# Optimization experiments

Hardware: AMD Instinct MI355X
Metric: run time of the kernel (lower is better)

The kernel has to match this reference:

```python
import jax, jax.numpy as jnp
import numpy as np

N, E, IN, H, D, C = 30000, 400000, 128, 4, 64, 40
EPS = 1e-5
SLOPE = 0.2  # DGL GATv2Conv leaky_relu negative_slope default


def setup_inputs() -> dict:
    key = jax.random.key(0)
    ks = jax.random.split(key, 20)
    def rn(k, shape, s=0.05):
        return jax.random.normal(k, shape, jnp.float32) * s
    return {
        "x": jax.random.normal(ks[0], (N, IN), jnp.float32),
        "src": jax.random.randint(ks[1], (E,), 0, N),
        "dst": jax.random.randint(ks[2], (E,), 0, N),
        # layer 0: in=128 -> heads*64 (residual projection since 128 != 256)
        "W_src0": rn(ks[3], (IN, H * D)), "W_dst0": rn(ks[4], (IN, H * D)),
        "b0": jnp.zeros((H * D,), jnp.float32), "attn0": rn(ks[5], (H, D)),
        "res_W0": rn(ks[6], (IN, H * D)),
        # layer 1: 256 -> heads*64 (identity residual since 256 == 256)
        "W_src1": rn(ks[7], (H * D, H * D)), "W_dst1": rn(ks[8], (H * D, H * D)),
        "b1": jnp.zeros((H * D,), jnp.float32), "attn1": rn(ks[9], (H, D)),
        # layer 2: 256 -> heads*40 (residual projection)
        "W_src2": rn(ks[10], (H * D, H * C)), "W_dst2": rn(ks[11], (H * D, H * C)),
        "b2": jnp.zeros((H * C,), jnp.float32), "attn2": rn(ks[12], (H, C)),
        "res_W2": rn(ks[13], (H * D, H * C)),
        # batchnorm affine params (training-mode batch stats)
        "g0": jnp.ones((H * D,), jnp.float32), "be0": jnp.zeros((H * D,), jnp.float32),
        "g1": jnp.ones((H * D,), jnp.float32), "be1": jnp.zeros((H * D,), jnp.float32),
    }


def gatv2_layer(h, src, dst, Wsrc, Wdst, b, attn, resW, out_dim, relu_act):
    # DGL GATv2Conv: score_e = attn . leaky_relu(fc_src(h)[u] + fc_dst(h)[v])
    n = h.shape[0]
    fs = (h @ Wsrc).reshape(n, H, out_dim)
    fd = (h @ Wdst).reshape(n, H, out_dim)
    e = jax.nn.leaky_relu(fs[src] + fd[dst], SLOPE)      # [E, H, out]
    score = jnp.einsum("ehd,hd->eh", e, attn)            # [E, H]
    # segment softmax over incoming edges of each dst node
    m = jax.ops.segment_max(score, dst, num_segments=n)
    m = jnp.where(jnp.isfinite(m), m, 0.0)               # zero in-degree safety
    ex = jnp.exp(score - m[dst])
    denom = jax.ops.segment_sum(ex, dst, num_segments=n)
    alpha = ex / jnp.maximum(denom, 1e-9)[dst]
    rst = jax.ops.segment_sum(alpha[:, :, None] * fs[src], dst, num_segments=n)
    res = (h @ resW).reshape(n, H, out_dim) if resW is not None else h.reshape(n, H, out_dim)
    rst = rst + res + b.reshape(1, H, out_dim)
    return jax.nn.relu(rst) if relu_act else rst


def batchnorm(h, g, be):
    mu = h.mean(0)
    var = h.var(0)  # biased variance, as torch BN uses for normalization
    return g * (h - mu) * jax.lax.rsqrt(var + EPS) + be


def reference(x, src, dst, W_src0, W_dst0, b0, attn0, res_W0, W_src1, W_dst1, b1, attn1, W_src2, W_dst2, b2, attn2, res_W2, g0, be0, g1, be1):
    h = gatv2_layer(x, src, dst, W_src0, W_dst0, b0, attn0, res_W0, D, True)
    h = jax.nn.relu(batchnorm(h.reshape(N, H * D), g0, be0))  # dropout = identity (eval)
    h = gatv2_layer(h, src, dst, W_src1, W_dst1, b1, attn1, None, D, True)
    h = jax.nn.relu(batchnorm(h.reshape(N, H * D), g1, be1))
    h = gatv2_layer(h, src, dst, W_src2, W_dst2, b2, attn2, res_W2, C, False)
    h = h.mean(1)  # mean over heads -> [N, C]
    return jax.nn.log_softmax(h, axis=-1)
```

## Files before the change

### kernel.cpp

```cpp
#include <hip/hip_runtime.h>
#include <hip/hip_bf16.h>
#include <math.h>

#define NN 30000
#define EE 400000
#define INP 128
#define HH 4
#define DD 64
#define CC 40
#define HD 256
#define HC 160
#define NBLK 118

typedef unsigned short ushort;
typedef __attribute__((ext_vector_type(8))) short s8v;
typedef __attribute__((ext_vector_type(4))) float f4v;


__device__ inline ushort bf16_of_float(float f) {
    __hip_bfloat16 b = __float2bfloat16(f);
    return *(ushort*)&b;
}
__device__ __forceinline__ float2 cvt2(unsigned d) {
    return make_float2(__uint_as_float(d << 16), __uint_as_float(d & 0xFFFF0000u));
}
__device__ __forceinline__ float b2f(ushort u) { return __uint_as_float(((unsigned)u) << 16); }

__device__ __forceinline__ float2 f2add(float2 a, float2 b){ return make_float2(a.x+b.x, a.y+b.y); }
__device__ __forceinline__ float2 f2mul(float2 a, float2 b){ return make_float2(a.x*b.x, a.y*b.y); }
__device__ __forceinline__ float2 f2muls(float2 a, float s){ return make_float2(a.x*s, a.y*s); }
__device__ __forceinline__ float2 f2max(float2 a, float2 b){ return make_float2(fmaxf(a.x,b.x), fmaxf(a.y,b.y)); }
__device__ __forceinline__ float2 f2fma(float2 a, float2 b, float2 c){
    return make_float2(__fmaf_rn(a.x,b.x,c.x), __fmaf_rn(a.y,b.y,c.y));
}

__device__ __forceinline__ void gld16(const void* g, void* l) {
    __builtin_amdgcn_global_load_lds((const __attribute__((address_space(1))) void*)g,
                                     (__attribute__((address_space(3))) void*)l, 16, 0, 0);
}

__device__ __forceinline__ float rowsum16(float x) {
    int t;
    t = __builtin_amdgcn_update_dpp(0, __float_as_int(x), 0x128, 0xF, 0xF, false); x += __int_as_float(t);
    t = __builtin_amdgcn_update_dpp(0, __float_as_int(x), 0x124, 0xF, 0xF, false); x += __int_as_float(t);
    t = __builtin_amdgcn_update_dpp(0, __float_as_int(x), 0x122, 0xF, 0xF, false); x += __int_as_float(t);
    t = __builtin_amdgcn_update_dpp(0, __float_as_int(x), 0x121, 0xF, 0xF, false); x += __int_as_float(t);
    return x;
}
__device__ __forceinline__ float rowmax16(float x) {
    int t;
    t = __builtin_amdgcn_update_dpp(0, __float_as_int(x), 0x128, 0xF, 0xF, false); x = fmaxf(x, __int_as_float(t));
    t = __builtin_amdgcn_update_dpp(0, __float_as_int(x), 0x124, 0xF, 0xF, false); x = fmaxf(x, __int_as_float(t));
    t = __builtin_amdgcn_update_dpp(0, __float_as_int(x), 0x122, 0xF, 0xF, false); x = fmaxf(x, __int_as_float(t));
    t = __builtin_amdgcn_update_dpp(0, __float_as_int(x), 0x121, 0xF, 0xF, false); x = fmaxf(x, __int_as_float(t));
    return x;
}

#define XB 3750
#define TB 1408
#define ZB 240

__global__ __launch_bounds__(256) void k_prep(const float* __restrict__ x, ushort* __restrict__ xc,
        const float* W0, const float* W1, const float* W2, const float* W3,
        const float* W4, const float* W5, const float* W6, const float* W7,
        ushort* bt0, ushort* bt1, ushort* bt2,
        int* __restrict__ zero_region,
        const float* b0, const float* a0, const float* b1, const float* a1,
        const float* b2, const float* a2, const float* g0, const float* be0,
        const float* g1, const float* be1, ushort* __restrict__ smallv) {
    int b = blockIdx.x, t = threadIdx.x;
    if (b < XB) {
        int i = b * 256 + t;
        if (i < NN * INP / 4) {
            float4 v = ((const float4*)x)[i];
            ushort4 o;
            o.x = bf16_of_float(v.x); o.y = bf16_of_float(v.y);
            o.z = bf16_of_float(v.z); o.w = bf16_of_float(v.w);
            ((ushort4*)xc)[i] = o;
        }
    } else if (b < XB + TB) {
        const float* Ws[8] = {W0, W1, W2, W3, W4, W5, W6, W7};
        int g = (b - XB) * 256 + t;
        if (g < 98304) {
            int seg = g >> 15, local = g & 32767;
            int n = local >> 7, k = local & 127;
            bt0[g] = bf16_of_float(Ws[seg][k * 256 + n]);
        } else if (g < 229376) {
            int gg = g - 98304;
            int seg = gg >> 16, local = gg & 65535;
            int n = local >> 8, k = local & 255;
            bt1[gg] = bf16_of_float(Ws[3 + seg][k * 256 + n]);
        } else if (g < 360448) {
            int gg = g - 229376;
            int n = gg >> 8, k = gg & 255;
            ushort val = 0;
            if (n < 480) {
                int seg = n / 160;
                int nn = n - seg * 160;
                val = bf16_of_float(Ws[5 + seg][k * 160 + nn]);
            }
            bt2[gg] = val;
        }
    } else if (b < XB + TB + ZB) {
        int i = (b - XB - TB) * 256 + t;
        if (i < 1024 + 2 * NN + 192) zero_region[i] = 0;
    } else {
        const float* ptrs[10] = {b0, a0, b1, a1, b2, a2, g0, be0, g1, be1};
        const int sz[10] = {256, 256, 256, 256, 160, 160, 256, 256, 256, 256};
        int off = 0;
        for (int j = 0; j < 10; j++) {
            if (t < sz[j]) smallv[off + t] = bf16_of_float(ptrs[j][t]);
            off += sz[j];
        }
    }
}


__global__ __launch_bounds__(256) void k_hist(const int* __restrict__ dst, int* __restrict__ cnt) {
    int e = blockIdx.x * 256 + threadIdx.x;
    if (e < EE) atomicAdd(&cnt[dst[e]], 1);
}

__global__ __launch_bounds__(256) void k_binbeg(const int* __restrict__ cnt, int* __restrict__ binCnt,
                                                int* __restrict__ beg, int* __restrict__ total) {
    __shared__ int lb[64];
    __shared__ int ss[256];
    __shared__ int base;
    int t = threadIdx.x;
    if (t < 64) lb[t] = 0;
    __syncthreads();
    int i = blockIdx.x * 256 + t;
    int c = (i < NN) ? cnt[i] : 0;
    if (i < NN) atomicAdd(&lb[63 - min(c, 63)], 1);
    ss[t] = c;
    __syncthreads();
    if (t < 64 && lb[t] > 0) atomicAdd(&binCnt[t], lb[t]);
    for (int o = 1; o < 256; o <<= 1) {
        int v = (t >= o) ? ss[t - o] : 0;
        __syncthreads();
        ss[t] += v;
        __syncthreads();
    }
    if (t == 255) base = atomicAdd(total, ss[255]);
    __syncthreads();
    if (i < NN) beg[i] = base + ss[t] - c;
}

__global__ __launch_bounds__(256) void k_orderscatter(const int* __restrict__ cnt, const int* __restrict__ binCnt,
                                                      int* __restrict__ binPos, int* __restrict__ order,
                                                      const int* __restrict__ src, const int* __restrict__ dst,
                                                      const int* __restrict__ beg, int* __restrict__ pos,
                                                      int* __restrict__ srcs) {
    int t = threadIdx.x;
    if (blockIdx.x < NBLK) {
        __shared__ int lb[64], lbase[64], bpre[64];
        if (t < 64) { lb[t] = 0; bpre[t] = binCnt[t]; }
        __syncthreads();
        int i = blockIdx.x * 256 + t;
        int bin = 0, rank = 0;
        if (i < NN) {
            bin = 63 - min(cnt[i], 63);
            rank = atomicAdd(&lb[bin], 1);
        }
        for (int o = 1; o < 64; o <<= 1) {
            int v = (t >= o && t < 64) ? bpre[t - o] : 0;
            __syncthreads();
            if (t < 64) bpre[t] += v;
            __syncthreads();
        }
        if (t < 64 && lb[t] > 0)
            lbase[t] = bpre[t] - binCnt[t] + atomicAdd(&binPos[t], lb[t]);
        __syncthreads();
        if (i < NN) order[lbase[bin] + rank] = i;
    } else {
        int e = (blockIdx.x - NBLK) * 256 + t;
        if (e < EE) {
            int d = dst[e];
            int p = atomicAdd(&pos[d], 1);
            srcs[beg[d] + p] = src[e];
        }
    }
}


template<int K, int SEGW, int NSEG>
__global__ __launch_bounds__(256) void k_gemm_tiled(const ushort* __restrict__ A,
                                                    const ushort* __restrict__ Bt,
                                                    ushort* __restrict__ o0, ushort* __restrict__ o1,
                                                    ushort* __restrict__ o2) {
    __shared__ ushort As[128 * 32];
    __shared__ ushort Bs[128 * 32];
    int t = threadIdx.x;
    int wave = t >> 6, lane = t & 63;
    int m = lane & 15, q = lane >> 4;
    int row0 = blockIdx.x * 128, col0 = blockIdx.y * 128;
    int wr = (wave >> 1) << 6, wc = (wave & 1) << 6;
    f4v acc[4][4] = {};
    int c1 = t, c2 = t + 256;
    int ar1 = min(row0 + (c1 >> 2), NN - 1);
    int ar2 = min(row0 + (c2 >> 2), NN - 1);
    const ushort* a1 = A + (size_t)ar1 * K + (c1 & 3) * 8;
    const ushort* a2 = A + (size_t)ar2 * K + (c2 & 3) * 8;
    const ushort* b1 = Bt + (size_t)(col0 + (c1 >> 2)) * K + (c1 & 3) * 8;
    const ushort* b2 = Bt + (size_t)(col0 + (c2 >> 2)) * K + (c2 & 3) * 8;
    int wbase = wave << 10;
    char* AsB = (char*)As;
    char* BsB = (char*)Bs;

#pragma unroll
    for (int kt = 0; kt < K; kt += 32) {
        __syncthreads();
        gld16(a1 + kt, AsB + wbase);
        gld16(a2 + kt, AsB + 4096 + wbase);
        gld16(b1 + kt, BsB + wbase);
        gld16(b2 + kt, BsB + 4096 + wbase);
        __syncthreads();
        s8v af[4], bg[4];
#pragma unroll
        for (int i = 0; i < 4; i++) af[i] = *(const s8v*)&As[(wr + i * 16 + m) * 32 + q * 8];
#pragma unroll
        for (int c = 0; c < 4; c++) bg[c] = *(const s8v*)&Bs[(wc + c * 16 + m) * 32 + q * 8];
#pragma unroll
        for (int i = 0; i < 4; i++)
#pragma unroll
            for (int c = 0; c < 4; c++)
                acc[i][c] = __builtin_amdgcn_mfma_f32_16x16x32_bf16(bg[c], af[i], acc[i][c], 0, 0, 0);
    }

#pragma unroll
    for (int c = 0; c < 4; c++) {
        int gcb = col0 + wc + c * 16;
        if (gcb < SEGW * NSEG) {
            int seg = gcb / SEGW;
            int colb = gcb - seg * SEGW + q * 4;
            ushort* op = seg == 0 ? o0 : (seg == 1 ? o1 : o2);
#pragma unroll
            for (int i = 0; i < 4; i++) {
                int gr = row0 + wr + i * 16 + m;
                if (gr < NN) {
                    ushort4 s4;
                    s4.x = bf16_of_float(acc[i][c][0]);
                    s4.y = bf16_of_float(acc[i][c][1]);
                    s4.z = bf16_of_float(acc[i][c][2]);
                    s4.w = bf16_of_float(acc[i][c][3]);
                    *(ushort4*)&op[(size_t)gr * SEGW + colb] = s4;
                }
            }
        }
    }
}


template<int DH, bool FINAL>
__global__ __launch_bounds__(256) void k_aggregate(const ushort* __restrict__ fs, const ushort* __restrict__ fd,
                                                   const ushort* __restrict__ res,
                                                   const ushort* __restrict__ attn,
                                                   const ushort* __restrict__ bias,
                                                   const int* __restrict__ beg, const int* __restrict__ cnt,
                                                   const int* __restrict__ srcs,
                                                   const int* __restrict__ order,
                                                   ushort* __restrict__ outb, float* __restrict__ outf) {
    constexpr int F = HH * DH;
    constexpr int JMAX = DH >> 2;
    int tt = threadIdx.x;
    int v = __builtin_amdgcn_readfirstlane(order[blockIdx.x * 4 + (tt >> 6)]);
    int lane = tt & 63;
    int h = lane >> 4, j = lane & 15;
    bool act = j < JMAX;
    unsigned off = h * DH + 4 * j;
    unsigned vbase = (unsigned)v * F + off;
    float2 fda = {0.f,0.f}, fdb = {0.f,0.f}, ava = {0.f,0.f}, avb = {0.f,0.f};
    if (act) {
        uint2 d = *(const uint2*)&fd[vbase];
        fda = cvt2(d.x); fdb = cvt2(d.y);
        uint2 a = *(const uint2*)&attn[off];
        const float LOG2E = 1.4426950408889634f;
        ava = f2muls(cvt2(a.x), LOG2E); avb = f2muls(cvt2(a.y), LOG2E);
    }
    float l = 0.f;
    float2 acca = {0.f,0.f}, accb = {0.f,0.f};
    int b0i = beg[v], end = b0i + cnt[v];

    auto ldrow = [&](int u, float2& ra, float2& rb) {
        ra = make_float2(0.f, 0.f); rb = make_float2(0.f, 0.f);
        if (act) {
            uint2 d = *(const uint2*)&fs[(unsigned)u * F + off];
            ra = cvt2(d.x); rb = cvt2(d.y);
        }
    };
    auto dotlr = [&](const float2& ra, const float2& rb) -> float {
        float2 t0 = f2add(ra, fda);
        float2 t1 = f2add(rb, fdb);
        t0 = f2max(t0, f2muls(t0, 0.2f));
        t1 = f2max(t1, f2muls(t1, 0.2f));
        float2 p2 = f2mul(ava, t0);
        p2 = f2fma(avb, t1, p2);
        return p2.x + p2.y;
    };
    auto quadc = [&](const float2& r0a, const float2& r0b, const float2& r1a, const float2& r1b,
                     const float2& r2a, const float2& r2b, const float2& r3a, const float2& r3b) {
        float p0 = rowsum16(dotlr(r0a, r0b));
        float p1 = rowsum16(dotlr(r1a, r1b));
        float p2 = rowsum16(dotlr(r2a, r2b));
        float p3 = rowsum16(dotlr(r3a, r3b));
        float w0 = exp2f(p0), w1 = exp2f(p1), w2 = exp2f(p2), w3 = exp2f(p3);
        l += (w0 + w1) + (w2 + w3);
        acca = f2fma(make_float2(w0, w0), r0a, acca);
        accb = f2fma(make_float2(w0, w0), r0b, accb);
        acca = f2fma(make_float2(w1, w1), r1a, acca);
        accb = f2fma(make_float2(w1, w1), r1b, accb);
        acca = f2fma(make_float2(w2, w2), r2a, acca);
        accb = f2fma(make_float2(w2, w2), r2b, accb);
        acca = f2fma(make_float2(w3, w3), r3a, acca);
        accb = f2fma(make_float2(w3, w3), r3b, accb);
    };

    int i = b0i;
    if (i + 3 < end) {
        int u0 = srcs[i], u1 = srcs[i+1], u2 = srcs[i+2], u3 = srcs[i+3];
        float2 r0a, r0b, r1a, r1b, r2a, r2b, r3a, r3b;
        ldrow(u0, r0a, r0b); ldrow(u1, r1a, r1b);
        ldrow(u2, r2a, r2b); ldrow(u3, r3a, r3b);
        for (i += 4; i + 3 < end; i += 4) {
            int n0 = srcs[i], n1 = srcs[i+1], n2 = srcs[i+2], n3 = srcs[i+3];
            float2 s0a, s0b, s1a, s1b, s2a, s2b, s3a, s3b;
            ldrow(n0, s0a, s0b); ldrow(n1, s1a, s1b);
            ldrow(n2, s2a, s2b); ldrow(n3, s3a, s3b);
            quadc(r0a, r0b, r1a, r1b, r2a, r2b, r3a, r3b);
            r0a = s0a; r0b = s0b; r1a = s1a; r1b = s1b;
            r2a = s2a; r2b = s2b; r3a = s3a; r3b = s3b;
        }
        quadc(r0a, r0b, r1a, r1b, r2a, r2b, r3a, r3b);
    }
    for (; i < end; i++) {
        float2 ra, rb;
        ldrow(srcs[i], ra, rb);
        float p0 = rowsum16(dotlr(ra, rb));
        float w0 = exp2f(p0);
        l += w0;
        acca = f2fma(make_float2(w0, w0), ra, acca);
        accb = f2fma(make_float2(w0, w0), rb, accb);
    }

    float4 o4 = {0.f, 0.f, 0.f, 0.f};
    if (act) {
        float inv = 1.f / fmaxf(l, 1e-9f);
        uint2 rr = *(const uint2*)&res[vbase];
        float2 rl = cvt2(rr.x), rh = cvt2(rr.y);
        uint2 bb = *(const uint2*)&bias[off];
        float2 bl = cvt2(bb.x), bh = cvt2(bb.y);
        o4.x = acca.x * inv + rl.x + bl.x;
        o4.y = acca.y * inv + rl.y + bl.y;
        o4.z = accb.x * inv + rh.x + bh.x;
        o4.w = accb.y * inv + rh.y + bh.y;
        if (!FINAL) {
            o4.x = fmaxf(o4.x, 0.f); o4.y = fmaxf(o4.y, 0.f);
            o4.z = fmaxf(o4.z, 0.f); o4.w = fmaxf(o4.w, 0.f);
        }
    }
    if (!FINAL) {
        if (act) {
            ushort4 s4;
            s4.x = bf16_of_float(o4.x); s4.y = bf16_of_float(o4.y);
            s4.z = bf16_of_float(o4.z); s4.w = bf16_of_float(o4.w);
            *(ushort4*)&outb[vbase] = s4;
        }
    } else {
#pragma unroll
        for (int msk = 16; msk <= 32; msk <<= 1) {
            o4.x += __shfl_xor(o4.x, msk, 64);
            o4.y += __shfl_xor(o4.y, msk, 64);
            o4.z += __shfl_xor(o4.z, msk, 64);
            o4.w += __shfl_xor(o4.w, msk, 64);
        }
        float4 zv = make_float4(0.25f * o4.x, 0.25f * o4.y, 0.25f * o4.z, 0.25f * o4.w);
        float mx4 = act ? fmaxf(fmaxf(zv.x, zv.y), fmaxf(zv.z, zv.w)) : -1e30f;
        float mx = rowmax16(mx4);
        float es = 0.f;
        if (act) es = __expf(zv.x - mx) + __expf(zv.y - mx) + __expf(zv.z - mx) + __expf(zv.w - mx);
        float ssum = rowsum16(es);
        float lse = mx + logf(ssum);
        if (act && h == 0) {
            float4 w4 = make_float4(zv.x - lse, zv.y - lse, zv.z - lse, zv.w - lse);
            *(float4*)&outf[(size_t)v * CC + 4 * j] = w4;
        }
    }
}


__global__ __launch_bounds__(256) void k_bn_partial(const ushort* __restrict__ h, float* __restrict__ sum,
                                                    float* __restrict__ sumsq) {
    int c = threadIdx.x;
    int r0 = blockIdx.x * 128;
    int r1 = min(NN, r0 + 128);
    float s0 = 0.f, ss0 = 0.f, s1 = 0.f, ss1 = 0.f;
    int r = r0;
#pragma unroll 4
    for (; r + 1 < r1; r += 2) {
        float v0 = b2f(h[(size_t)r * HD + c]);
        float v1 = b2f(h[(size_t)(r + 1) * HD + c]);
        s0 += v0; ss0 = __fmaf_rn(v0, v0, ss0);
        s1 += v1; ss1 = __fmaf_rn(v1, v1, ss1);
    }
    if (r < r1) {
        float v0 = b2f(h[(size_t)r * HD + c]);
        s0 += v0; ss0 = __fmaf_rn(v0, v0, ss0);
    }
    atomicAdd(&sum[c], s0 + s1);
    atomicAdd(&sumsq[c], ss0 + ss1);
}


__global__ __launch_bounds__(256) void k_bn_norm(const ushort* __restrict__ hin, const float* __restrict__ sum,
                                                 const float* __restrict__ sumsq,
                                                 const ushort* __restrict__ g,
                                                 const ushort* __restrict__ be,
                                                 ushort* __restrict__ hbf) {
    int i4 = blockIdx.x * 256 + threadIdx.x;
    if (i4 < NN * HD / 4) {
        int base = i4 * 4;
        int c = base & (HD - 1);
        ushort4 hv = ((const ushort4*)hin)[i4];
        ushort4 ov;
        float vv[4] = {b2f(hv.x), b2f(hv.y), b2f(hv.z), b2f(hv.w)};
        ushort* po = (ushort*)&ov;
#pragma unroll
        for (int k = 0; k < 4; k++) {
            float mean = sum[c + k] * (1.0f / NN);
            float var = fmaxf(sumsq[c + k] * (1.0f / NN) - mean * mean, 0.f);
            float y = b2f(g[c + k]) * (vv[k] - mean) * rsqrtf(var + 1e-5f) + b2f(be[c + k]);
            po[k] = bf16_of_float(fmaxf(y, 0.f));
        }
        ((ushort4*)hbf)[i4] = ov;
    }
}


static inline char* alignup(char* p) { return (char*)(((size_t)p + 255) & ~(size_t)255); }

extern "C" void kernel_launch(void* const* d_in, const int* in_sizes, int n_in,
                              void* d_out, int out_size, void* d_ws, size_t ws_size,
                              hipStream_t stream) {
    const float* x     = (const float*)d_in[0];
    const int*  src    = (const int*)d_in[1];
    const int*  dst    = (const int*)d_in[2];
    const float* Wsrc0 = (const float*)d_in[3];
    const float* Wdst0 = (const float*)d_in[4];
    const float* b0    = (const float*)d_in[5];
    const float* attn0 = (const float*)d_in[6];
    const float* resW0 = (const float*)d_in[7];
    const float* Wsrc1 = (const float*)d_in[8];
    const float* Wdst1 = (const float*)d_in[9];
    const float* b1    = (const float*)d_in[10];
    const float* attn1 = (const float*)d_in[11];
    const float* Wsrc2 = (const float*)d_in[12];
    const float* Wdst2 = (const float*)d_in[13];
    const float* b2    = (const float*)d_in[14];
    const float* attn2 = (const float*)d_in[15];
    const float* resW2 = (const float*)d_in[16];
    const float* g0    = (const float*)d_in[17];
    const float* be0   = (const float*)d_in[18];
    const float* g1    = (const float*)d_in[19];
    const float* be1   = (const float*)d_in[20];

    char* w = (char*)d_ws;
    const size_t NF = (size_t)NN * HD;
    ushort* fsb = (ushort*)w; w += NF * 2;
    ushort* fdb = (ushort*)w; w += NF * 2;
    ushort* resb= (ushort*)w; w += NF * 2;
    ushort* hag = (ushort*)w; w += NF * 2;
    ushort* hbf = (ushort*)w; w += NF * 2;
    ushort* xc  = (ushort*)w; w += (size_t)NN * INP * 2;
    ushort* bt0 = (ushort*)w; w += 768 * 128 * 2;
    ushort* bt1 = (ushort*)w; w += 512 * 256 * 2;
    ushort* bt2 = (ushort*)w; w += 512 * 256 * 2;
    ushort* smallv = (ushort*)w; w += 2368 * 2; w = alignup(w);
    float* bnstats = (float*)w; w += 1024 * 4;
    int* cnt    = (int*)w; w += NN * 4;
    int* pos    = (int*)w; w += NN * 4;
    int* binCnt = (int*)w; w += 64 * 4;
    int* binPos = (int*)w; w += 64 * 4;
    int* total  = (int*)w; w += 64 * 4; w = alignup(w);
    int* beg    = (int*)w; w += NN * 4; w = alignup(w);
    int* order  = (int*)w; w += NN * 4; w = alignup(w);
    int* srcs   = (int*)w; w += EE * 4;

    const ushort* c_b0    = smallv + 0;
    const ushort* c_attn0 = smallv + 256;
    const ushort* c_b1    = smallv + 512;
    const ushort* c_attn1 = smallv + 768;
    const ushort* c_b2    = smallv + 1024;
    const ushort* c_attn2 = smallv + 1184;
    const ushort* c_g0    = smallv + 1344;
    const ushort* c_be0   = smallv + 1600;
    const ushort* c_g1    = smallv + 1856;
    const ushort* c_be1   = smallv + 2112;

    k_prep<<<XB + TB + ZB + 1, 256, 0, stream>>>(x, xc,
        Wsrc0, Wdst0, resW0, Wsrc1, Wdst1, Wsrc2, Wdst2, resW2, bt0, bt1, bt2,
        (int*)bnstats,
        b0, attn0, b1, attn1, b2, attn2, g0, be0, g1, be1, smallv);

    k_hist<<<(EE + 255) / 256, 256, 0, stream>>>(dst, cnt);
    k_binbeg<<<NBLK, 256, 0, stream>>>(cnt, binCnt, beg, total);
    k_orderscatter<<<NBLK + (EE + 255) / 256, 256, 0, stream>>>(cnt, binCnt, binPos, order,
                                                                src, dst, beg, pos, srcs);

    const int MB = (NN + 127) / 128;

    k_gemm_tiled<128, 256, 3><<<dim3(MB, 6), 256, 0, stream>>>(xc, bt0, fsb, fdb, resb);
    k_aggregate<DD, false><<<NN / 4, 256, 0, stream>>>(fsb, fdb, resb, c_attn0, c_b0,
        beg, cnt, srcs, order, hag, nullptr);
    k_bn_partial<<<MB, 256, 0, stream>>>(hag, bnstats, bnstats + 256);
    k_bn_norm<<<(int)((NF / 4 + 255) / 256), 256, 0, stream>>>(hag, bnstats, bnstats + 256,
                                                               c_g0, c_be0, hbf);

    k_gemm_tiled<256, 256, 2><<<dim3(MB, 4), 256, 0, stream>>>(hbf, bt1, fsb, fdb, nullptr);
    k_aggregate<DD, false><<<NN / 4, 256, 0, stream>>>(fsb, fdb, hbf, c_attn1, c_b1,
        beg, cnt, srcs, order, hag, nullptr);
    k_bn_partial<<<MB, 256, 0, stream>>>(hag, bnstats + 512, bnstats + 768);
    k_bn_norm<<<(int)((NF / 4 + 255) / 256), 256, 0, stream>>>(hag, bnstats + 512, bnstats + 768,
                                                               c_g1, c_be1, hbf);

    k_gemm_tiled<256, 160, 3><<<dim3(MB, 4), 256, 0, stream>>>(hbf, bt2, fsb, fdb, resb);
    k_aggregate<CC, true><<<NN / 4, 256, 0, stream>>>(fsb, fdb, resb, c_attn2, c_b2,
        beg, cnt, srcs, order, nullptr, (float*)d_out);
}
```

Measured before the change: 358.7 us.

## Double-buffer GEMM LDS tiles and use native float2 vector ops in aggregation

The tiled GEMM now keeps two LDS buffers, prefetching the next K-slice with global_load_lds while MFMAs consume the current one, so there is one barrier per iteration instead of two. The aggregation kernel switches from hand-written float2 structs to ext_vector_type float2 with elementwise fma/max builtins, so the compiler can emit packed FP32 instructions. This doubles GEMM LDS use, which may lower occupancy. The GEMM K loop is short (K=128 or 256), which limits how much overlap is possible.

Result: no change. 361.4 us (+0.7%).

```diff
diff --git a/kernel.cpp b/kernel.cpp
--- a/kernel.cpp
+++ b/kernel.cpp
@@ -15,23 +15,35 @@
 typedef unsigned short ushort;
 typedef __attribute__((ext_vector_type(8))) short s8v;
 typedef __attribute__((ext_vector_type(4))) float f4v;
+typedef __attribute__((ext_vector_type(2))) float f2;
 
 
 __device__ inline ushort bf16_of_float(float f) {
     __hip_bfloat16 b = __float2bfloat16(f);
     return *(ushort*)&b;
 }
-__device__ __forceinline__ float2 cvt2(unsigned d) {
-    return make_float2(__uint_as_float(d << 16), __uint_as_float(d & 0xFFFF0000u));
-}
 __device__ __forceinline__ float b2f(ushort u) { return __uint_as_float(((unsigned)u) << 16); }
 
-__device__ __forceinline__ float2 f2add(float2 a, float2 b){ return make_float2(a.x+b.x, a.y+b.y); }
-__device__ __forceinline__ float2 f2mul(float2 a, float2 b){ return make_float2(a.x*b.x, a.y*b.y); }
-__device__ __forceinline__ float2 f2muls(float2 a, float s){ return make_float2(a.x*s, a.y*s); }
-__device__ __forceinline__ float2 f2max(float2 a, float2 b){ return make_float2(fmaxf(a.x,b.x), fmaxf(a.y,b.y)); }
-__device__ __forceinline__ float2 f2fma(float2 a, float2 b, float2 c){
-    return make_float2(__fmaf_rn(a.x,b.x,c.x), __fmaf_rn(a.y,b.y,c.y));
+__device__ __forceinline__ f2 cvt2v(unsigned d) {
+    f2 r;
+    r.x = __uint_as_float(d << 16);
+    r.y = __uint_as_float(d & 0xFFFF0000u);
+    return r;
+}
+__device__ __forceinline__ f2 splat2(float s) { f2 r = {s, s}; return r; }
+__device__ __forceinline__ f2 f2fmav(f2 a, f2 b, f2 c) {
+#if __has_builtin(__builtin_elementwise_fma)
+    return __builtin_elementwise_fma(a, b, c);
+#else
+    f2 r; r.x = __fmaf_rn(a.x, b.x, c.x); r.y = __fmaf_rn(a.y, b.y, c.y); return r;
+#endif
+}
+__device__ __forceinline__ f2 f2maxv(f2 a, f2 b) {
+#if __has_builtin(__builtin_elementwise_max)
+    return __builtin_elementwise_max(a, b);
+#else
+    f2 r; r.x = fmaxf(a.x, b.x); r.y = fmaxf(a.y, b.y); return r;
+#endif
 }
 
 __device__ __forceinline__ void gld16(const void* g, void* l) {
@@ -188,8 +200,8 @@
                                                     const ushort* __restrict__ Bt,
                                                     ushort* __restrict__ o0, ushort* __restrict__ o1,
                                                     ushort* __restrict__ o2) {
-    __shared__ ushort As[128 * 32];
-    __shared__ ushort Bs[128 * 32];
+    __shared__ ushort As[2 * 128 * 32];
+    __shared__ ushort Bs[2 * 128 * 32];
     int t = threadIdx.x;
     int wave = t >> 6, lane = t & 63;
     int m = lane & 15, q = lane >> 4;
@@ -207,24 +219,34 @@
     char* AsB = (char*)As;
     char* BsB = (char*)Bs;
 
+    gld16(a1, AsB + wbase);
+    gld16(a2, AsB + 4096 + wbase);
+    gld16(b1, BsB + wbase);
+    gld16(b2, BsB + 4096 + wbase);
+    __syncthreads();
+
 #pragma unroll
     for (int kt = 0; kt < K; kt += 32) {
-        __syncthreads();
-        gld16(a1 + kt, AsB + wbase);
-        gld16(a2 + kt, AsB + 4096 + wbase);
-        gld16(b1 + kt, BsB + wbase);
-        gld16(b2 + kt, BsB + 4096 + wbase);
-        __syncthreads();
+        int cur = (kt >> 5) & 1;
+        int curo = cur * 4096;
+        if (kt + 32 < K) {
+            int nb = (cur ^ 1) * 8192;
+            gld16(a1 + kt + 32, AsB + nb + wbase);
+            gld16(a2 + kt + 32, AsB + nb + 4096 + wbase);
+            gld16(b1 + kt + 32, BsB + nb + wbase);
+            gld16(b2 + kt + 32, BsB + nb + 4096 + wbase);
+        }
         s8v af[4], bg[4];
 #pragma unroll
-        for (int i = 0; i < 4; i++) af[i] = *(const s8v*)&As[(wr + i * 16 + m) * 32 + q * 8];
-#pragma unroll
-        for (int c = 0; c < 4; c++) bg[c] = *(const s8v*)&Bs[(wc + c * 16 + m) * 32 + q * 8];
+        for (int i = 0; i < 4; i++) af[i] = *(const s8v*)&As[curo + (wr + i * 16 + m) * 32 + q * 8];
+#pragma unroll
+        for (int c = 0; c < 4; c++) bg[c] = *(const s8v*)&Bs[curo + (wc + c * 16 + m) * 32 + q * 8];
 #pragma unroll
         for (int i = 0; i < 4; i++)
 #pragma unroll
             for (int c = 0; c < 4; c++)
                 acc[i][c] = __builtin_amdgcn_mfma_f32_16x16x32_bf16(bg[c], af[i], acc[i][c], 0, 0, 0);
+        if (kt + 32 < K) __syncthreads();
     }
 
 #pragma unroll
@@ -269,61 +291,61 @@
     bool act = j < JMAX;
     unsigned off = h * DH + 4 * j;
     unsigned vbase = (unsigned)v * F + off;
-    float2 fda = {0.f,0.f}, fdb = {0.f,0.f}, ava = {0.f,0.f}, avb = {0.f,0.f};
+    f2 fda = {0.f, 0.f}, fdb = {0.f, 0.f}, ava = {0.f, 0.f}, avb = {0.f, 0.f};
     if (act) {
         uint2 d = *(const uint2*)&fd[vbase];
-        fda = cvt2(d.x); fdb = cvt2(d.y);
+        fda = cvt2v(d.x); fdb = cvt2v(d.y);
         uint2 a = *(const uint2*)&attn[off];
         const float LOG2E = 1.4426950408889634f;
-        ava = f2muls(cvt2(a.x), LOG2E); avb = f2muls(cvt2(a.y), LOG2E);
+        ava = cvt2v(a.x) * LOG2E; avb = cvt2v(a.y) * LOG2E;
     }
     float l = 0.f;
-    float2 acca = {0.f,0.f}, accb = {0.f,0.f};
+    f2 acca = {0.f, 0.f}, accb = {0.f, 0.f};
     int b0i = beg[v], end = b0i + cnt[v];
 
-    auto ldrow = [&](int u, float2& ra, float2& rb) {
-        ra = make_float2(0.f, 0.f); rb = make_float2(0.f, 0.f);
+    auto ldrow = [&](int u, f2& ra, f2& rb) {
+        ra = splat2(0.f); rb = splat2(0.f);
         if (act) {
             uint2 d = *(const uint2*)&fs[(unsigned)u * F + off];
-            ra = cvt2(d.x); rb = cvt2(d.y);
+            ra = cvt2v(d.x); rb = cvt2v(d.y);
         }
     };
-    auto dotlr = [&](const float2& ra, const float2& rb) -> float {
-        float2 t0 = f2add(ra, fda);
-        float2 t1 = f2add(rb, fdb);
-        t0 = f2max(t0, f2muls(t0, 0.2f));
-        t1 = f2max(t1, f2muls(t1, 0.2f));
-        float2 p2 = f2mul(ava, t0);
-        p2 = f2fma(avb, t1, p2);
+    auto dotlr = [&](const f2& ra, const f2& rb) -> float {
+        f2 t0 = ra + fda;
+        f2 t1 = rb + fdb;
+        t0 = f2maxv(t0, t0 * 0.2f);
+        t1 = f2maxv(t1, t1 * 0.2f);
+        f2 p2 = ava * t0;
+        p2 = f2fmav(avb, t1, p2);
         return p2.x + p2.y;
     };
-    auto quadc = [&](const float2& r0a, const float2& r0b, const float2& r1a, const float2& r1b,
-                     const float2& r2a, const float2& r2b, const float2& r3a, const float2& r3b) {
+    auto quadc = [&](const f2& r0a, const f2& r0b, const f2& r1a, const f2& r1b,
+                     const f2& r2a, const f2& r2b, const f2& r3a, const f2& r3b) {
         float p0 = rowsum16(dotlr(r0a, r0b));
         float p1 = rowsum16(dotlr(r1a, r1b));
         float p2 = rowsum16(dotlr(r2a, r2b));
         float p3 = rowsum16(dotlr(r3a, r3b));
         float w0 = exp2f(p0), w1 = exp2f(p1), w2 = exp2f(p2), w3 = exp2f(p3);
         l += (w0 + w1) + (w2 + w3);
-        acca = f2fma(make_float2(w0, w0), r0a, acca);
-        accb = f2fma(make_float2(w0, w0), r0b, accb);
-        acca = f2fma(make_float2(w1, w1), r1a, acca);
-        accb = f2fma(make_float2(w1, w1), r1b, accb);
-        acca = f2fma(make_float2(w2, w2), r2a, acca);
-        accb = f2fma(make_float2(w2, w2), r2b, accb);
-        acca = f2fma(make_float2(w3, w3), r3a, acca);
-        accb = f2fma(make_float2(w3, w3), r3b, accb);
+        acca = f2fmav(splat2(w0), r0a, acca);
+        accb = f2fmav(splat2(w0), r0b, accb);
+        acca = f2fmav(splat2(w1), r1a, acca);
+        accb = f2fmav(splat2(w1), r1b, accb);
+        acca = f2fmav(splat2(w2), r2a, acca);
+        accb = f2fmav(splat2(w2), r2b, accb);
+        acca = f2fmav(splat2(w3), r3a, acca);
+        accb = f2fmav(splat2(w3), r3b, accb);
     };
 
     int i = b0i;
     if (i + 3 < end) {
         int u0 = srcs[i], u1 = srcs[i+1], u2 = srcs[i+2], u3 = srcs[i+3];
-        float2 r0a, r0b, r1a, r1b, r2a, r2b, r3a, r3b;
+        f2 r0a, r0b, r1a, r1b, r2a, r2b, r3a, r3b;
         ldrow(u0, r0a, r0b); ldrow(u1, r1a, r1b);
         ldrow(u2, r2a, r2b); ldrow(u3, r3a, r3b);
         for (i += 4; i + 3 < end; i += 4) {
             int n0 = srcs[i], n1 = srcs[i+1], n2 = srcs[i+2], n3 = srcs[i+3];
-            float2 s0a, s0b, s1a, s1b, s2a, s2b, s3a, s3b;
+            f2 s0a, s0b, s1a, s1b, s2a, s2b, s3a, s3b;
             ldrow(n0, s0a, s0b); ldrow(n1, s1a, s1b);
             ldrow(n2, s2a, s2b); ldrow(n3, s3a, s3b);
             quadc(r0a, r0b, r1a, r1b, r2a, r2b, r3a, r3b);
@@ -333,22 +355,22 @@
         quadc(r0a, r0b, r1a, r1b, r2a, r2b, r3a, r3b);
     }
     for (; i < end; i++) {
-        float2 ra, rb;
+        f2 ra, rb;
         ldrow(srcs[i], ra, rb);
         float p0 = rowsum16(dotlr(ra, rb));
         float w0 = exp2f(p0);
         l += w0;
-        acca = f2fma(make_float2(w0, w0), ra, acca);
-        accb = f2fma(make_float2(w0, w0), rb, accb);
+        acca = f2fmav(splat2(w0), ra, acca);
+        accb = f2fmav(splat2(w0), rb, accb);
     }
 
     float4 o4 = {0.f, 0.f, 0.f, 0.f};
     if (act) {
         float inv = 1.f / fmaxf(l, 1e-9f);
         uint2 rr = *(const uint2*)&res[vbase];
-        float2 rl = cvt2(rr.x), rh = cvt2(rr.y);
+        f2 rl = cvt2v(rr.x), rh = cvt2v(rr.y);
         uint2 bb = *(const uint2*)&bias[off];
-        float2 bl = cvt2(bb.x), bh = cvt2(bb.y);
+        f2 bl = cvt2v(bb.x), bh = cvt2v(bb.y);
         o4.x = acca.x * inv + rl.x + bl.x;
         o4.y = acca.y * inv + rl.y + bl.y;
         o4.z = accb.x * inv + rh.x + bh.x;
```
